# Optimization experiments

Hardware: AMD Instinct MI355X
Metric: run time of the kernel (lower is better)

The kernel has to match this reference:

```python
import jax, jax.numpy as jnp
import numpy as np

HIDDEN = 2048
HEADS = 16
HEAD_DIM = HIDDEN // HEADS  # 128
ROPE_BASE = 10000.0
RMS_EPS = 1e-6
MINUS_INF = -10000.0


def rms_norm(x, w):
    xf = x.astype(jnp.float32)
    var = jnp.mean(xf * xf, axis=-1, keepdims=True)
    return w * (x * jax.lax.rsqrt(var + RMS_EPS))


def rotate_half(x):
    x1, x2 = jnp.split(x, 2, axis=-1)
    return jnp.concatenate((-x2, x1), axis=-1)


def rope_tables(seq_len, dtype):
    inv_freq = 1.0 / (ROPE_BASE ** (jnp.arange(0, HEAD_DIM, 2, dtype=jnp.float32) / HEAD_DIM))
    t = jnp.arange(seq_len, dtype=jnp.float32)
    freqs = jnp.einsum('i,j->ij', t, inv_freq)           # [S, D/2]
    emb = jnp.concatenate((freqs, freqs), axis=-1)       # [S, D]
    return jnp.cos(emb).astype(dtype), jnp.sin(emb).astype(dtype)


def setup_inputs() -> dict:
    key = jax.random.key(0)
    ks = jax.random.split(key, 6)
    B, S, H = 2, 2048, HIDDEN
    x = jax.random.normal(ks[0], (B, S, H), dtype=jnp.float32) * 0.5
    norm_w = jnp.ones((H,), dtype=jnp.float32)
    scale = 0.02
    wq = jax.random.normal(ks[1], (H, H), dtype=jnp.float32) * scale
    wk = jax.random.normal(ks[2], (H, H), dtype=jnp.float32) * scale
    wv = jax.random.normal(ks[3], (H, H), dtype=jnp.float32) * scale
    wo = jax.random.normal(ks[4], (H, H), dtype=jnp.float32) * scale
    position_ids = jnp.broadcast_to(jnp.arange(S, dtype=jnp.int32), (B, S))
    return {"x": x, "norm_w": norm_w, "wq": wq, "wk": wk, "wv": wv,
            "wo": wo, "position_ids": position_ids}


def reference(x, norm_w, wq, wk, wv, wo, position_ids):
    B, S, H = x.shape
    h = rms_norm(x, norm_w)
    # torch Linear: y = h @ W.T, weight is [out, in]
    def proj(w):
        return jnp.einsum('bsd,od->bso', h, w).reshape(B, S, HEADS, HEAD_DIM).transpose(0, 2, 1, 3)
    q, k, v = proj(wq), proj(wk), proj(wv)  # [B, Hh, S, D]
    cos, sin = rope_tables(S, x.dtype)
    cos = cos[position_ids][:, None]  # [B, 1, S, D]
    sin = sin[position_ids][:, None]
    q = q * cos + rotate_half(q) * sin
    k = k * cos + rotate_half(k) * sin
    scores = jnp.einsum('bhqd,bhkd->bhqk', q, k) / jnp.sqrt(jnp.float32(HEAD_DIM))
    causal = jnp.tril(jnp.ones((S, S), dtype=bool))
    scores = scores + jnp.where(causal, 0.0, MINUS_INF).astype(scores.dtype)
    probs = jax.nn.softmax(scores, axis=-1)
    ctx = jnp.einsum('bhqk,bhkd->bhqd', probs, v)          # [B, Hh, S, D]
    ctx = ctx.transpose(0, 2, 1, 3).reshape(B, S, H)
    out = jnp.einsum('bsd,od->bso', ctx, wo)
    return out
```

## Files before the change

kernel.cpp:

```cpp
#include <hip/hip_runtime.h>
#include <hip/hip_bf16.h>
#include <stdint.h>

#define S_LEN   2048
#define BATCH   2
#define HID     2048
#define NHEADS  16
#define HDIM    128
#define ROWS    (BATCH * S_LEN)
#define QS      6144
#define ATT_SCALE 0.08838834764831843f
#define LOG2E     1.4426950408889634f

typedef __attribute__((ext_vector_type(8))) short s16x8;
typedef __attribute__((ext_vector_type(4))) float f32x4;

#define GLL16(gp, lp)                                                          \
  __builtin_amdgcn_global_load_lds(                                            \
      (__attribute__((address_space(1))) void*)(gp),                           \
      (__attribute__((address_space(3))) void*)(lp), 16, 0, 0)

__device__ __forceinline__ float bf2f(unsigned short u) {
  union { unsigned int i; float f; } v; v.i = ((unsigned int)u) << 16; return v.f;
}
__device__ __forceinline__ unsigned short f2bf(float f) {
  union { float f; unsigned int i; } v; v.f = f;
  unsigned int i = v.i;
  return (unsigned short)((i + 0x7FFFu + ((i >> 16) & 1u)) >> 16);
}
__device__ __forceinline__ void store_out(unsigned short* p, float v) { *p = f2bf(v); }
__device__ __forceinline__ void store_out(float* p, float v) { *p = v; }

__global__ __launch_bounds__(256) void cast4_kernel(const float* __restrict__ w0,
                                                    const float* __restrict__ w1,
                                                    const float* __restrict__ w2,
                                                    const float* __restrict__ w3,
                                                    unsigned short* __restrict__ dqkv,
                                                    unsigned short* __restrict__ dwo) {
  const int which = blockIdx.y;
  const float* src = (which == 0) ? w0 : (which == 1) ? w1 : (which == 2) ? w2 : w3;
  unsigned short* dst = (which < 3) ? dqkv + (size_t)which * HID * HID : dwo;
  int i = blockIdx.x * 256 + threadIdx.x;
  float4 v = ((const float4*)src)[i];
  ushort4 o;
  o.x = f2bf(v.x); o.y = f2bf(v.y); o.z = f2bf(v.z); o.w = f2bf(v.w);
  ((ushort4*)dst)[i] = o;
}

__global__ __launch_bounds__(256) void rmsnorm_kernel(const float* __restrict__ x,
                                                      const float* __restrict__ w,
                                                      unsigned short* __restrict__ h) {
  int row = blockIdx.x;
  int t = threadIdx.x;
  const float4* xr4 = (const float4*)(x + (size_t)row * HID);
  float4 a = xr4[t], b = xr4[t + 256];
  float ss = a.x*a.x + a.y*a.y + a.z*a.z + a.w*a.w
           + b.x*b.x + b.y*b.y + b.z*b.z + b.w*b.w;
#pragma unroll
  for (int off = 32; off >= 1; off >>= 1) ss += __shfl_xor(ss, off, 64);
  __shared__ float red[4];
  if ((t & 63) == 0) red[t >> 6] = ss;
  __syncthreads();
  float tot = red[0] + red[1] + red[2] + red[3];
  float rs = rsqrtf(tot * (1.0f / (float)HID) + 1e-6f);
  const float4* w4 = (const float4*)w;
  float4 wa = w4[t], wb = w4[t + 256];
  ushort4 oa, ob;
  oa.x = f2bf(a.x * wa.x * rs); oa.y = f2bf(a.y * wa.y * rs);
  oa.z = f2bf(a.z * wa.z * rs); oa.w = f2bf(a.w * wa.w * rs);
  ob.x = f2bf(b.x * wb.x * rs); ob.y = f2bf(b.y * wb.y * rs);
  ob.z = f2bf(b.z * wb.z * rs); ob.w = f2bf(b.w * wb.w * rs);
  ushort4* hr = (ushort4*)(h + (size_t)row * HID);
  hr[t] = oa; hr[t + 256] = ob;
}

__global__ void rope_tab_kernel(float* __restrict__ cost, float* __restrict__ sint) {
  int s = blockIdx.x, j = threadIdx.x;
  float inv = powf(10000.0f, -((float)j) / 64.0f);
  float ang = (float)s * inv;
  cost[s * 64 + j] = cosf(ang);
  sint[s * 64 + j] = sinf(ang);
}

__global__ __launch_bounds__(256) void rope_kernel(const int* __restrict__ pos_ids,
                                                   const float* __restrict__ cost,
                                                   const float* __restrict__ sint,
                                                   unsigned short* __restrict__ qkv) {
  int row = blockIdx.x;
  int p = pos_ids[row];
  int t = threadIdx.x;
  int head = t >> 4;
  int j0 = (t & 15) * 4;
  size_t base = (size_t)row * QS + head * HDIM;
  float4 c = *(const float4*)(cost + p * 64 + j0);
  float4 s = *(const float4*)(sint + p * 64 + j0);
#pragma unroll
  for (int which = 0; which < 2; which++) {
    unsigned short* ptr = qkv + base + which * HID;
    float sc = which ? 1.0f : (ATT_SCALE * LOG2E);
    ushort4 v1 = *(ushort4*)(ptr + j0);
    ushort4 v2 = *(ushort4*)(ptr + 64 + j0);
    ushort4 o1, o2;
    o1.x = f2bf((bf2f(v1.x) * c.x - bf2f(v2.x) * s.x) * sc);
    o1.y = f2bf((bf2f(v1.y) * c.y - bf2f(v2.y) * s.y) * sc);
    o1.z = f2bf((bf2f(v1.z) * c.z - bf2f(v2.z) * s.z) * sc);
    o1.w = f2bf((bf2f(v1.w) * c.w - bf2f(v2.w) * s.w) * sc);
    o2.x = f2bf((bf2f(v2.x) * c.x + bf2f(v1.x) * s.x) * sc);
    o2.y = f2bf((bf2f(v2.y) * c.y + bf2f(v1.y) * s.y) * sc);
    o2.z = f2bf((bf2f(v2.z) * c.z + bf2f(v1.z) * s.z) * sc);
    o2.w = f2bf((bf2f(v2.w) * c.w + bf2f(v1.w) * s.w) * sc);
    *(ushort4*)(ptr + j0) = o1;
    *(ushort4*)(ptr + 64 + j0) = o2;
  }
}

__global__ __launch_bounds__(256) void transpose_v_kernel(const unsigned short* __restrict__ qkv,
                                                          unsigned short* __restrict__ vt) {
  __shared__ unsigned short tile[64][72];
  const int stile = blockIdx.x, dt = blockIdx.y, bh = blockIdx.z;
  const int t = threadIdx.x;
  const int b = bh >> 4, h = bh & 15;
  const int s0 = stile * 64;
  const unsigned short* src = qkv + (size_t)(b * S_LEN + s0) * QS + 2 * HID + h * HDIM + dt * 64;
#pragma unroll
  for (int it = 0; it < 2; it++) {
    int sl = (t >> 3) + 32 * it;
    int dl = (t & 7) * 8;
    *(s16x8*)&tile[sl][dl] = *(const s16x8*)(src + (size_t)sl * QS + dl);
  }
  __syncthreads();
#pragma unroll
  for (int it = 0; it < 2; it++) {
    int dl = (t >> 3) + 32 * it;
    int sl8 = (t & 7) * 8;
    s16x8 o;
#pragma unroll
    for (int jj = 0; jj < 8; jj++) o[jj] = (short)tile[sl8 + jj][dl];
    *(s16x8*)(vt + (size_t)(bh * 128 + dt * 64 + dl) * S_LEN + s0 + sl8) = o;
  }
}

#define SH(kt, bi, kk2) {                                                      \
    const unsigned short* sa_ = aQ + (size_t)(kt) * 64 + (kk2) * 32;           \
    const unsigned short* sb_ = bQ + (size_t)(kt) * 64 + (kk2) * 32;           \
    char* da_ = qsm + ((bi) * 2 + (kk2)) * 32768 + tid * 16;                   \
    GLL16(sa_, da_);                                                           \
    GLL16(sa_ + (size_t)128 * K, da_ + 8192);                                  \
    GLL16(sb_, da_ + 16384);                                                   \
    GLL16(sb_ + (size_t)128 * K, da_ + 16384 + 8192);                          \
  }

__global__ __launch_bounds__(512, 2) void gemm_qk_kernel(const unsigned short* __restrict__ A,
                                                         const unsigned short* __restrict__ B,
                                                         unsigned short* __restrict__ C,
                                                         int K, int N) {
  __shared__ __align__(16) unsigned short Qsm[2][2][2][256 * 32];
  const int bm = blockIdx.y, bn = blockIdx.x;
  const int tid = threadIdx.x;
  const int w = tid >> 6, wr = w >> 2, wc = w & 3;
  const int l = tid & 63, g = l >> 4, r = l & 15;
  const int KT = K >> 6;

  const int srow = tid >> 2;
  const int sg = (tid & 3) ^ ((tid >> 2) & 3) ^ ((tid >> 4) & 3);
  const unsigned short* aQ = A + (size_t)(bm * 256 + srow) * K + sg * 8;
  const unsigned short* bQ = B + (size_t)(bn * 256 + srow) * K + sg * 8;
  char* const qsm = (char*)Qsm;

  f32x4 zero = {0.f, 0.f, 0.f, 0.f};
  f32x4 acc[8][4];
#pragma unroll
  for (int mi = 0; mi < 8; mi++)
#pragma unroll
    for (int ni = 0; ni < 4; ni++) acc[mi][ni] = zero;

  const int ro = ((g ^ (r & 3) ^ ((r >> 2) & 3)) << 4);
  const int aOff = (wr * 128 + r) * 64 + ro;
  const int bOff = 16384 + (wc * 64 + r) * 64 + ro;

  SH(0, 0, 0); SH(0, 0, 1);

  for (int kt = 0; kt < KT; ++kt) {
    const int buf = kt & 1;
    const bool more = (kt + 1 < KT);
    const char* l0 = qsm + (buf * 2 + 0) * 32768;
    const char* l1 = qsm + (buf * 2 + 1) * 32768;

    asm volatile("s_waitcnt vmcnt(4)" ::: "memory");
    __builtin_amdgcn_s_barrier();
    __builtin_amdgcn_sched_barrier(0);
    s16x8 a[4], b[4];
#pragma unroll
    for (int ni = 0; ni < 4; ni++) b[ni] = *(const s16x8*)(l0 + bOff + ni * 1024);
#pragma unroll
    for (int i = 0; i < 4; i++) a[i] = *(const s16x8*)(l0 + aOff + i * 1024);
    if (more) SH(kt + 1, buf ^ 1, 0);
    __builtin_amdgcn_s_setprio(1);
#pragma unroll
    for (int ni = 0; ni < 4; ni++)
#pragma unroll
      for (int i = 0; i < 4; i++)
        acc[i][ni] = __builtin_amdgcn_mfma_f32_16x16x32_bf16(a[i], b[ni], acc[i][ni], 0, 0, 0);
    __builtin_amdgcn_s_setprio(0);

    s16x8 a2[4];
#pragma unroll
    for (int i = 0; i < 4; i++) a2[i] = *(const s16x8*)(l0 + aOff + (4 + i) * 1024);
    __builtin_amdgcn_s_setprio(1);
#pragma unroll
    for (int ni = 0; ni < 4; ni++)
#pragma unroll
      for (int i = 0; i < 4; i++)
        acc[4 + i][ni] = __builtin_amdgcn_mfma_f32_16x16x32_bf16(a2[i], b[ni], acc[4 + i][ni], 0, 0, 0);
    __builtin_amdgcn_s_setprio(0);

    if (more) { asm volatile("s_waitcnt vmcnt(4)" ::: "memory"); }
    else      { asm volatile("s_waitcnt vmcnt(0)" ::: "memory"); }
    __builtin_amdgcn_s_barrier();
    __builtin_amdgcn_sched_barrier(0);
#pragma unroll
    for (int ni = 0; ni < 4; ni++) b[ni] = *(const s16x8*)(l1 + bOff + ni * 1024);
#pragma unroll
    for (int i = 0; i < 4; i++) a[i] = *(const s16x8*)(l1 + aOff + i * 1024);
    if (more) SH(kt + 1, buf ^ 1, 1);
    __builtin_amdgcn_s_setprio(1);
#pragma unroll
    for (int ni = 0; ni < 4; ni++)
#pragma unroll
      for (int i = 0; i < 4; i++)
        acc[i][ni] = __builtin_amdgcn_mfma_f32_16x16x32_bf16(a[i], b[ni], acc[i][ni], 0, 0, 0);
    __builtin_amdgcn_s_setprio(0);

#pragma unroll
    for (int i = 0; i < 4; i++) a2[i] = *(const s16x8*)(l1 + aOff + (4 + i) * 1024);
    __builtin_amdgcn_s_setprio(1);
#pragma unroll
    for (int ni = 0; ni < 4; ni++)
#pragma unroll
      for (int i = 0; i < 4; i++)
        acc[4 + i][ni] = __builtin_amdgcn_mfma_f32_16x16x32_bf16(a2[i], b[ni], acc[4 + i][ni], 0, 0, 0);
    __builtin_amdgcn_s_setprio(0);
  }

#pragma unroll
  for (int mi = 0; mi < 8; mi++)
#pragma unroll
    for (int ni = 0; ni < 4; ni++) {
      const int crow = bm * 256 + wr * 128 + mi * 16 + g * 4;
      const int ccol = bn * 256 + wc * 64 + ni * 16 + r;
#pragma unroll
      for (int j = 0; j < 4; j++)
        store_out(&C[(size_t)(crow + j) * N + ccol], acc[mi][ni][j]);
    }
}
#undef SH

#define SA(kt, bi) {                                                           \
    const unsigned short* s_ = aS + (size_t)(kt) * 64;                         \
    char* d_ = (char*)Ab[bi] + tid * 16;                                       \
    GLL16(s_, d_);                                                             \
    GLL16(s_ + (size_t)64 * K, d_ + 8192);                                     \
  }
#define SB(kt, bi, hf) {                                                       \
    const unsigned short* s_ = bS + (size_t)(hf) * 128 * K + (size_t)(kt) * 64;\
    char* d_ = (char*)Bb[bi] + (hf) * 16384 + tid * 16;                        \
    GLL16(s_, d_);                                                             \
    GLL16(s_ + (size_t)64 * K, d_ + 8192);                                     \
  }

template <typename OutT, int NI>
__global__ __launch_bounds__(512, 1) void gemm8_kernel(const unsigned short* __restrict__ A,
                                                       const unsigned short* __restrict__ B,
                                                       OutT* __restrict__ C, int K, int N) {
  __shared__ __align__(16) unsigned short Ab[3][128 * 64];
  __shared__ __align__(16) unsigned short Bb[3][NI * 64 * 64];
  const int bm = blockIdx.y, bn = blockIdx.x;
  const int tid = threadIdx.x;
  const int w = tid >> 6, wr = w >> 2, wc = w & 3;
  const int l = tid & 63, g = l >> 4, r = l & 15;
  const int KT = K >> 6;

  const int srow = tid >> 3;
  const int sgr = (tid & 7) ^ (srow & 7);
  const unsigned short* aS = A + (size_t)(bm * 128 + srow) * K + sgr * 8;
  const unsigned short* bS = B + (size_t)(bn * (NI * 64) + srow) * K + sgr * 8;

  f32x4 zero = {0.f, 0.f, 0.f, 0.f};
  f32x4 acc[4][NI];
#pragma unroll
  for (int mi = 0; mi < 4; mi++)
#pragma unroll
    for (int ni = 0; ni < NI; ni++) acc[mi][ni] = zero;

  const int swx = (r & 7) << 4;
  const int ks0 = (g << 4) ^ swx;
  const int ks1 = ((4 | g) << 4) ^ swx;
  const int aOff = (wr * 64 + r) * 128;
  const int bOff = (wc * (NI * 16) + r) * 128;

  SA(0, 0); SB(0, 0, 0); if (NI == 4) SB(0, 0, 1);
  SA(1, 1); SB(1, 1, 0); if (NI == 4) SB(1, 1, 1);

  int cur = 0;
  for (int kt = 0; kt < KT; ++kt) {
    const int b2 = (cur >= 1) ? cur - 1 : cur + 2;
    if (kt == KT - 1)      { asm volatile("s_waitcnt vmcnt(0)" ::: "memory"); }
    else if (NI == 4)      { asm volatile("s_waitcnt vmcnt(6)" ::: "memory"); }
    else                   { asm volatile("s_waitcnt vmcnt(4)" ::: "memory"); }
    __builtin_amdgcn_s_barrier();
    __builtin_amdgcn_sched_barrier(0);
    const char* lA = (const char*)Ab[cur];
    const char* lB = (const char*)Bb[cur];
    const bool more = (kt + 2 < KT);

    s16x8 a[4][2], b[NI][2];
#pragma unroll
    for (int mi = 0; mi < 4; mi++) {
      a[mi][0] = *(const s16x8*)(lA + aOff + mi * 2048 + ks0);
      a[mi][1] = *(const s16x8*)(lA + aOff + mi * 2048 + ks1);
    }
#pragma unroll
    for (int ni = 0; ni < NI / 2; ni++) {
      b[ni][0] = *(const s16x8*)(lB + bOff + ni * 2048 + ks0);
      b[ni][1] = *(const s16x8*)(lB + bOff + ni * 2048 + ks1);
    }
    if (more) { SA(kt + 2, b2); if (NI == 4) SB(kt + 2, b2, 0); }
    __builtin_amdgcn_s_setprio(1);
#pragma unroll
    for (int kk = 0; kk < 2; kk++)
#pragma unroll
      for (int ni = 0; ni < NI / 2; ni++)
#pragma unroll
        for (int mi = 0; mi < 4; mi++)
          acc[mi][ni] = __builtin_amdgcn_mfma_f32_16x16x32_bf16(a[mi][kk], b[ni][kk], acc[mi][ni], 0, 0, 0);
    __builtin_amdgcn_s_setprio(0);
    __builtin_amdgcn_sched_barrier(0);

#pragma unroll
    for (int ni = NI / 2; ni < NI; ni++) {
      b[ni][0] = *(const s16x8*)(lB + bOff + ni * 2048 + ks0);
      b[ni][1] = *(const s16x8*)(lB + bOff + ni * 2048 + ks1);
    }
    if (more) { if (NI == 4) { SB(kt + 2, b2, 1); } else { SB(kt + 2, b2, 0); } }
    __builtin_amdgcn_s_setprio(1);
#pragma unroll
    for (int kk = 0; kk < 2; kk++)
#pragma unroll
      for (int ni = NI / 2; ni < NI; ni++)
#pragma unroll
        for (int mi = 0; mi < 4; mi++)
          acc[mi][ni] = __builtin_amdgcn_mfma_f32_16x16x32_bf16(a[mi][kk], b[ni][kk], acc[mi][ni], 0, 0, 0);
    __builtin_amdgcn_s_setprio(0);
    cur = (cur == 2) ? 0 : cur + 1;
  }

#pragma unroll
  for (int mi = 0; mi < 4; mi++)
#pragma unroll
    for (int ni = 0; ni < NI; ni++) {
      const int crow = bm * 128 + wr * 64 + mi * 16 + g * 4;
      const int ccol = bn * (NI * 64) + wc * (NI * 16) + ni * 16 + r;
#pragma unroll
      for (int j = 0; j < 4; j++)
        store_out(&C[(size_t)(crow + j) * N + ccol], acc[mi][ni][j]);
    }
}

__global__ __launch_bounds__(256, 2) void attn_kernel(const unsigned short* __restrict__ QKV,
                                                      const unsigned short* __restrict__ VT,
                                                      unsigned short* __restrict__ O) {
  __shared__ __align__(16) unsigned short Ksm[2][64 * 128];
  __shared__ __align__(16) unsigned short VTsm[2][128 * 64];
  __shared__ __align__(16) unsigned short Psm[4 * 16 * 64];
  const int bid = blockIdx.x;
  const int grp = bid & 7, idx = bid >> 3;
  const int qt = 31 - (idx >> 2);
  const int bh = (grp << 2) | (idx & 3);
  const int b = bh >> 4, hd = bh & 15;
  const int tid = threadIdx.x, w = tid >> 6, l = tid & 63, g = l >> 4, r = l & 15;
  const int qbs = qt * 64 + w * 16;

  const unsigned short* qp = QKV + (size_t)(b * S_LEN + qbs + r) * QS + hd * HDIM;
  s16x8 qf[4];
#pragma unroll
  for (int ks = 0; ks < 4; ks++) qf[ks] = *(const s16x8*)(qp + ks * 32 + g * 8);

  float mreg[4], lreg[4];
  f32x4 zero = {0.f, 0.f, 0.f, 0.f};
  f32x4 oacc[8];
#pragma unroll
  for (int jj = 0; jj < 4; jj++) { mreg[jj] = -1e30f; lreg[jj] = 0.f; }
#pragma unroll
  for (int di = 0; di < 8; di++) oacc[di] = zero;

  const int cK = tid & 15, rowK = tid >> 4;
  const unsigned short* kp_base = QKV + (size_t)(b * S_LEN + rowK) * QS + HID + hd * HDIM
                                  + ((cK ^ (rowK & 7)) << 3);
  const int cV = tid & 7, dV = tid >> 3;
  const unsigned short* vp_base = VT + (size_t)(bh * 128 + dV) * S_LEN + ((cV ^ (dV & 7)) << 3);
  char* const ksm0 = (char*)Ksm;
  char* const vtsm0 = (char*)VTsm;
  char* const psm_w = (char*)Psm + w * 2048;

#define STAGE(kt, bufi)                                                        \
  {                                                                            \
    const unsigned short* kp_ = kp_base + (size_t)((kt) * 64) * QS;            \
    const unsigned short* vp_ = vp_base + (kt) * 64;                           \
    char* kd_ = ksm0 + (bufi) * 16384;                                         \
    char* vd_ = vtsm0 + (bufi) * 16384;                                        \
    GLL16(kp_,                      kd_ + tid * 16);                           \
    GLL16(kp_ + (size_t)16 * QS,    kd_ + (tid + 256) * 16);                   \
    GLL16(kp_ + (size_t)32 * QS,    kd_ + (tid + 512) * 16);                   \
    GLL16(kp_ + (size_t)48 * QS,    kd_ + (tid + 768) * 16);                   \
    GLL16(vp_,                      vd_ + tid * 16);                           \
    GLL16(vp_ + (size_t)32 * S_LEN, vd_ + (tid + 256) * 16);                   \
    GLL16(vp_ + (size_t)64 * S_LEN, vd_ + (tid + 512) * 16);                   \
    GLL16(vp_ + (size_t)96 * S_LEN, vd_ + (tid + 768) * 16);                   \
  }

  const int nt = qt + 1;
  STAGE(0, 0);

  for (int kt2 = 0; kt2 < nt; kt2++) {
    const int buf = kt2 & 1;
    asm volatile("s_waitcnt vmcnt(0)" ::: "memory");
    __builtin_amdgcn_s_barrier();
    __builtin_amdgcn_sched_barrier(0);
    if (kt2 + 1 < nt) STAGE(kt2 + 1, buf ^ 1);

    const char* ksm_c = ksm0 + buf * 16384;
    const char* vtsm_c = vtsm0 + buf * 16384;

    f32x4 sacc[4];
#pragma unroll
    for (int ni = 0; ni < 4; ni++) sacc[ni] = zero;
#pragma unroll
    for (int ni = 0; ni < 4; ni++) {
      const int krow = ni * 16 + r;
      const int swz = (krow & 7) << 4;
      const char* kb2 = ksm_c + krow * 256;
#pragma unroll
      for (int ks = 0; ks < 4; ks++) {
        s16x8 kf = *(const s16x8*)(kb2 + ((ks * 64 + g * 16) ^ swz));
        sacc[ni] = __builtin_amdgcn_mfma_f32_16x16x32_bf16(qf[ks], kf, sacc[ni], 0, 0, 0);
      }
    }

    if (kt2 == qt) {
#pragma unroll
      for (int ni = 0; ni < 4; ni++)
#pragma unroll
        for (int jj = 0; jj < 4; jj++)
          if ((kt2 * 64 + ni * 16 + r) > (qbs + g * 4 + jj)) sacc[ni][jj] = -1e30f;
    }

    float mrow[4];
#pragma unroll
    for (int jj = 0; jj < 4; jj++)
      mrow[jj] = fmaxf(fmaxf(sacc[0][jj], sacc[1][jj]), fmaxf(sacc[2][jj], sacc[3][jj]));
#pragma unroll
    for (int jj = 0; jj < 4; jj++) {
#pragma unroll
      for (int off = 8; off >= 1; off >>= 1)
        mrow[jj] = fmaxf(mrow[jj], __shfl_xor(mrow[jj], off, 64));
    }
    bool grow = false;
#pragma unroll
    for (int jj = 0; jj < 4; jj++) grow = grow || (mrow[jj] > mreg[jj] + 8.0f);
    if (__any(grow)) {
#pragma unroll
      for (int jj = 0; jj < 4; jj++) {
        float mn = fmaxf(mreg[jj], mrow[jj]);
        float corr = exp2f(mreg[jj] - mn);
        mreg[jj] = mn;
        lreg[jj] *= corr;
#pragma unroll
        for (int di = 0; di < 8; di++) oacc[di][jj] *= corr;
      }
    }
#pragma unroll
    for (int jj = 0; jj < 4; jj++) {
      float sm = 0.f;
#pragma unroll
      for (int ni = 0; ni < 4; ni++) {
        float p2 = exp2f(sacc[ni][jj] - mreg[jj]);
        sacc[ni][jj] = p2;
        sm += p2;
      }
#pragma unroll
      for (int off = 8; off >= 1; off >>= 1) sm += __shfl_xor(sm, off, 64);
      lreg[jj] += sm;
    }

#pragma unroll
    for (int ni = 0; ni < 4; ni++) {
      unsigned int pk01, pk23;
      asm("v_cvt_pk_bf16_f32 %0, %1, %2" : "=v"(pk01) : "v"(sacc[ni][0]), "v"(sacc[ni][1]));
      asm("v_cvt_pk_bf16_f32 %0, %1, %2" : "=v"(pk23) : "v"(sacc[ni][2]), "v"(sacc[ni][3]));
      const int col2 = (ni * 16 + r) << 1;
      const int pr0 = g * 4;
      *(unsigned short*)(psm_w + (((pr0 + 0) * 128 + col2) ^ (((pr0 + 0) & 7) << 4))) = (unsigned short)pk01;
      *(unsigned short*)(psm_w + (((pr0 + 1) * 128 + col2) ^ (((pr0 + 1) & 7) << 4))) = (unsigned short)(pk01 >> 16);
      *(unsigned short*)(psm_w + (((pr0 + 2) * 128 + col2) ^ (((pr0 + 2) & 7) << 4))) = (unsigned short)pk23;
      *(unsigned short*)(psm_w + (((pr0 + 3) * 128 + col2) ^ (((pr0 + 3) & 7) << 4))) = (unsigned short)(pk23 >> 16);
    }

#pragma unroll
    for (int ksl = 0; ksl < 2; ksl++) {
      s16x8 pa = *(const s16x8*)(psm_w + ((r * 128 + ((ksl * 32 + g * 8) << 1)) ^ ((r & 7) << 4)));
      const int kgran = ksl * 4 + g;
#pragma unroll
      for (int di = 0; di < 8; di++) {
        const int d = di * 16 + r;
        s16x8 vf = *(const s16x8*)(vtsm_c + d * 128 + ((kgran ^ (d & 7)) << 4));
        oacc[di] = __builtin_amdgcn_mfma_f32_16x16x32_bf16(pa, vf, oacc[di], 0, 0, 0);
      }
    }
  }
#undef STAGE

#pragma unroll
  for (int di = 0; di < 8; di++)
#pragma unroll
    for (int jj = 0; jj < 4; jj++) {
      int orow = qbs + g * 4 + jj;
      O[(size_t)(b * S_LEN + orow) * HID + hd * HDIM + di * 16 + r] =
          f2bf(oacc[di][jj] / lreg[jj]);
    }
}

extern "C" void kernel_launch(void* const* d_in, const int* in_sizes, int n_in,
                              void* d_out, int out_size, void* d_ws, size_t ws_size,
                              hipStream_t stream) {
  const float* x      = (const float*)d_in[0];
  const float* norm_w = (const float*)d_in[1];
  const float* wq     = (const float*)d_in[2];
  const float* wk     = (const float*)d_in[3];
  const float* wv     = (const float*)d_in[4];
  const float* wo     = (const float*)d_in[5];
  const int*   pos    = (const int*)d_in[6];
  float* out = (float*)d_out;

  char* ws = (char*)d_ws;
  const size_t WQKV_B = (size_t)3 * HID * HID * 2;
  const size_t WO_B   = (size_t)HID * HID * 2;
  const size_t H_B    = (size_t)ROWS * HID * 2;
  const size_t QKV_B  = (size_t)ROWS * QS * 2;

  unsigned short* wqkvb = (unsigned short*)(ws);
  unsigned short* vt    = (unsigned short*)(ws);
  unsigned short* wob   = (unsigned short*)(ws + WQKV_B);
  unsigned short* h     = (unsigned short*)(ws + WQKV_B + WO_B);
  unsigned short* qkv   = (unsigned short*)(ws + WQKV_B + WO_B + H_B);
  float* cost = (float*)(ws + WQKV_B + WO_B + H_B + QKV_B);
  float* sint = cost + (size_t)S_LEN * 64;

  dim3 cgrid(HID * HID / 4 / 256, 4);
  cast4_kernel<<<cgrid, 256, 0, stream>>>(wq, wk, wv, wo, wqkvb, wob);
  rope_tab_kernel<<<S_LEN, 64, 0, stream>>>(cost, sint);
  rmsnorm_kernel<<<ROWS, 256, 0, stream>>>(x, norm_w, h);

  dim3 qkgrid(2 * HID / 256, ROWS / 256);
  gemm_qk_kernel<<<qkgrid, 512, 0, stream>>>(h, wqkvb, qkv, HID, QS);

  dim3 vgrid(HID / 256, ROWS / 128);
  gemm8_kernel<unsigned short, 4><<<vgrid, 512, 0, stream>>>(
      h, wqkvb + (size_t)2 * HID * HID, qkv + 2 * HID, HID, QS);

  dim3 tgrid(S_LEN / 64, 2, BATCH * NHEADS);
  transpose_v_kernel<<<tgrid, 256, 0, stream>>>(qkv, vt);

  rope_kernel<<<ROWS, 256, 0, stream>>>(pos, cost, sint, qkv);

  attn_kernel<<<1024, 256, 0, stream>>>(qkv, vt, h );

  dim3 ogrid(HID / 256, ROWS / 128);
  gemm8_kernel<float, 4><<<ogrid, 512, 0, stream>>>(h, wob, out, HID, HID);
}
```

Measured before the change: 284.6 us.

## Fuse V transpose into V GEMM epilogue and transpose attention MFMA layout

The V projection GEMM now writes its output directly in the transposed [b,h,d,s] layout, which removes the separate transpose kernel and the round trip of V through the QKV buffer. The QKV buffer shrinks to Q and K only. The attention kernel swaps MFMA operand order so each lane owns one query row. That lets row max and row sum reductions use two shuffles and one scalar per lane instead of four, makes P writes into shared memory packed 32-bit stores, and makes output stores vectorized. The cost is that the V GEMM epilogue writes scattered 8-byte stores, and V now overlaps the weight buffer in the workspace, so ordering across kernels matters.

```diff
diff --git a/kernel.cpp b/kernel.cpp
--- a/kernel.cpp
+++ b/kernel.cpp
@@ -8,7 +8,7 @@
 #define NHEADS  16
 #define HDIM    128
 #define ROWS    (BATCH * S_LEN)
-#define QS      6144
+#define QKS     4096
 #define ATT_SCALE 0.08838834764831843f
 #define LOG2E     1.4426950408889634f
 
@@ -85,18 +85,18 @@
 __global__ __launch_bounds__(256) void rope_kernel(const int* __restrict__ pos_ids,
                                                    const float* __restrict__ cost,
                                                    const float* __restrict__ sint,
-                                                   unsigned short* __restrict__ qkv) {
+                                                   unsigned short* __restrict__ qk) {
   int row = blockIdx.x;
   int p = pos_ids[row];
   int t = threadIdx.x;
   int head = t >> 4;
   int j0 = (t & 15) * 4;
-  size_t base = (size_t)row * QS + head * HDIM;
+  size_t base = (size_t)row * QKS + head * HDIM;
   float4 c = *(const float4*)(cost + p * 64 + j0);
   float4 s = *(const float4*)(sint + p * 64 + j0);
 #pragma unroll
   for (int which = 0; which < 2; which++) {
-    unsigned short* ptr = qkv + base + which * HID;
+    unsigned short* ptr = qk + base + which * HID;
     float sc = which ? 1.0f : (ATT_SCALE * LOG2E);
     ushort4 v1 = *(ushort4*)(ptr + j0);
     ushort4 v2 = *(ushort4*)(ptr + 64 + j0);
@@ -114,32 +114,6 @@
   }
 }
 
-__global__ __launch_bounds__(256) void transpose_v_kernel(const unsigned short* __restrict__ qkv,
-                                                          unsigned short* __restrict__ vt) {
-  __shared__ unsigned short tile[64][72];
-  const int stile = blockIdx.x, dt = blockIdx.y, bh = blockIdx.z;
-  const int t = threadIdx.x;
-  const int b = bh >> 4, h = bh & 15;
-  const int s0 = stile * 64;
-  const unsigned short* src = qkv + (size_t)(b * S_LEN + s0) * QS + 2 * HID + h * HDIM + dt * 64;
-#pragma unroll
-  for (int it = 0; it < 2; it++) {
-    int sl = (t >> 3) + 32 * it;
-    int dl = (t & 7) * 8;
-    *(s16x8*)&tile[sl][dl] = *(const s16x8*)(src + (size_t)sl * QS + dl);
-  }
-  __syncthreads();
-#pragma unroll
-  for (int it = 0; it < 2; it++) {
-    int dl = (t >> 3) + 32 * it;
-    int sl8 = (t & 7) * 8;
-    s16x8 o;
-#pragma unroll
-    for (int jj = 0; jj < 8; jj++) o[jj] = (short)tile[sl8 + jj][dl];
-    *(s16x8*)(vt + (size_t)(bh * 128 + dt * 64 + dl) * S_LEN + s0 + sl8) = o;
-  }
-}
-
 #define SH(kt, bi, kk2) {                                                      \
     const unsigned short* sa_ = aQ + (size_t)(kt) * 64 + (kk2) * 32;           \
     const unsigned short* sb_ = bQ + (size_t)(kt) * 64 + (kk2) * 32;           \
@@ -268,7 +242,7 @@
     GLL16(s_ + (size_t)64 * K, d_ + 8192);                                     \
   }
 
-template <typename OutT, int NI>
+template <typename OutT, int NI, bool VT_OUT>
 __global__ __launch_bounds__(512, 1) void gemm8_kernel(const unsigned short* __restrict__ A,
                                                        const unsigned short* __restrict__ B,
                                                        OutT* __restrict__ C, int K, int N) {
@@ -360,13 +334,23 @@
     for (int ni = 0; ni < NI; ni++) {
       const int crow = bm * 128 + wr * 64 + mi * 16 + g * 4;
       const int ccol = bn * (NI * 64) + wc * (NI * 16) + ni * 16 + r;
-#pragma unroll
-      for (int j = 0; j < 4; j++)
-        store_out(&C[(size_t)(crow + j) * N + ccol], acc[mi][ni][j]);
-    }
-}
-
-__global__ __launch_bounds__(256, 2) void attn_kernel(const unsigned short* __restrict__ QKV,
+      if constexpr (VT_OUT) {
+        const int bidx = crow >> 11;
+        const int s0 = crow & (S_LEN - 1);
+        const int vrow = (bidx * 16 + (ccol >> 7)) * 128 + (ccol & 127);
+        ushort4 o;
+        o.x = f2bf(acc[mi][ni][0]); o.y = f2bf(acc[mi][ni][1]);
+        o.z = f2bf(acc[mi][ni][2]); o.w = f2bf(acc[mi][ni][3]);
+        *(ushort4*)((unsigned short*)C + (size_t)vrow * S_LEN + s0) = o;
+      } else {
+#pragma unroll
+        for (int j = 0; j < 4; j++)
+          store_out(&C[(size_t)(crow + j) * N + ccol], acc[mi][ni][j]);
+      }
+    }
+}
+
+__global__ __launch_bounds__(256, 2) void attn_kernel(const unsigned short* __restrict__ QK,
                                                       const unsigned short* __restrict__ VT,
                                                       unsigned short* __restrict__ O) {
   __shared__ __align__(16) unsigned short Ksm[2][64 * 128];
@@ -380,38 +364,37 @@
   const int tid = threadIdx.x, w = tid >> 6, l = tid & 63, g = l >> 4, r = l & 15;
   const int qbs = qt * 64 + w * 16;
 
-  const unsigned short* qp = QKV + (size_t)(b * S_LEN + qbs + r) * QS + hd * HDIM;
+  const unsigned short* qp = QK + (size_t)(b * S_LEN + qbs + r) * QKS + hd * HDIM;
   s16x8 qf[4];
 #pragma unroll
   for (int ks = 0; ks < 4; ks++) qf[ks] = *(const s16x8*)(qp + ks * 32 + g * 8);
 
-  float mreg[4], lreg[4];
+  float mreg = -1e30f, lreg = 0.f;
   f32x4 zero = {0.f, 0.f, 0.f, 0.f};
   f32x4 oacc[8];
 #pragma unroll
-  for (int jj = 0; jj < 4; jj++) { mreg[jj] = -1e30f; lreg[jj] = 0.f; }
-#pragma unroll
   for (int di = 0; di < 8; di++) oacc[di] = zero;
 
   const int cK = tid & 15, rowK = tid >> 4;
-  const unsigned short* kp_base = QKV + (size_t)(b * S_LEN + rowK) * QS + HID + hd * HDIM
+  const unsigned short* kp_base = QK + (size_t)(b * S_LEN + rowK) * QKS + HID + hd * HDIM
                                   + ((cK ^ (rowK & 7)) << 3);
   const int cV = tid & 7, dV = tid >> 3;
   const unsigned short* vp_base = VT + (size_t)(bh * 128 + dV) * S_LEN + ((cV ^ (dV & 7)) << 3);
   char* const ksm0 = (char*)Ksm;
   char* const vtsm0 = (char*)VTsm;
   char* const psm_w = (char*)Psm + w * 2048;
+  const int pswz = (r & 7) << 4;
 
 #define STAGE(kt, bufi)                                                        \
   {                                                                            \
-    const unsigned short* kp_ = kp_base + (size_t)((kt) * 64) * QS;            \
+    const unsigned short* kp_ = kp_base + (size_t)((kt) * 64) * QKS;           \
     const unsigned short* vp_ = vp_base + (kt) * 64;                           \
     char* kd_ = ksm0 + (bufi) * 16384;                                         \
     char* vd_ = vtsm0 + (bufi) * 16384;                                        \
     GLL16(kp_,                      kd_ + tid * 16);                           \
-    GLL16(kp_ + (size_t)16 * QS,    kd_ + (tid + 256) * 16);                   \
-    GLL16(kp_ + (size_t)32 * QS,    kd_ + (tid + 512) * 16);                   \
-    GLL16(kp_ + (size_t)48 * QS,    kd_ + (tid + 768) * 16);                   \
+    GLL16(kp_ + (size_t)16 * QKS,   kd_ + (tid + 256) * 16);                   \
+    GLL16(kp_ + (size_t)32 * QKS,   kd_ + (tid + 512) * 16);                   \
+    GLL16(kp_ + (size_t)48 * QKS,   kd_ + (tid + 768) * 16);                   \
     GLL16(vp_,                      vd_ + tid * 16);                           \
     GLL16(vp_ + (size_t)32 * S_LEN, vd_ + (tid + 256) * 16);                   \
     GLL16(vp_ + (size_t)64 * S_LEN, vd_ + (tid + 512) * 16);                   \
@@ -442,7 +425,7 @@
 #pragma unroll
       for (int ks = 0; ks < 4; ks++) {
         s16x8 kf = *(const s16x8*)(kb2 + ((ks * 64 + g * 16) ^ swz));
-        sacc[ni] = __builtin_amdgcn_mfma_f32_16x16x32_bf16(qf[ks], kf, sacc[ni], 0, 0, 0);
+        sacc[ni] = __builtin_amdgcn_mfma_f32_16x16x32_bf16(kf, qf[ks], sacc[ni], 0, 0, 0);
       }
     }
 
@@ -451,82 +434,72 @@
       for (int ni = 0; ni < 4; ni++)
 #pragma unroll
         for (int jj = 0; jj < 4; jj++)
-          if ((kt2 * 64 + ni * 16 + r) > (qbs + g * 4 + jj)) sacc[ni][jj] = -1e30f;
-    }
-
-    float mrow[4];
-#pragma unroll
-    for (int jj = 0; jj < 4; jj++)
-      mrow[jj] = fmaxf(fmaxf(sacc[0][jj], sacc[1][jj]), fmaxf(sacc[2][jj], sacc[3][jj]));
-#pragma unroll
-    for (int jj = 0; jj < 4; jj++) {
-#pragma unroll
-      for (int off = 8; off >= 1; off >>= 1)
-        mrow[jj] = fmaxf(mrow[jj], __shfl_xor(mrow[jj], off, 64));
-    }
-    bool grow = false;
-#pragma unroll
-    for (int jj = 0; jj < 4; jj++) grow = grow || (mrow[jj] > mreg[jj] + 8.0f);
-    if (__any(grow)) {
-#pragma unroll
-      for (int jj = 0; jj < 4; jj++) {
-        float mn = fmaxf(mreg[jj], mrow[jj]);
-        float corr = exp2f(mreg[jj] - mn);
-        mreg[jj] = mn;
-        lreg[jj] *= corr;
-#pragma unroll
-        for (int di = 0; di < 8; di++) oacc[di][jj] *= corr;
-      }
-    }
-#pragma unroll
-    for (int jj = 0; jj < 4; jj++) {
-      float sm = 0.f;
-#pragma unroll
-      for (int ni = 0; ni < 4; ni++) {
-        float p2 = exp2f(sacc[ni][jj] - mreg[jj]);
-        sacc[ni][jj] = p2;
-        sm += p2;
-      }
-#pragma unroll
-      for (int off = 8; off >= 1; off >>= 1) sm += __shfl_xor(sm, off, 64);
-      lreg[jj] += sm;
-    }
+          if ((kt2 * 64 + ni * 16 + g * 4 + jj) > (qbs + r)) sacc[ni][jj] = -1e30f;
+    }
+
+    float m0 = fmaxf(fmaxf(sacc[0][0], sacc[0][1]), fmaxf(sacc[0][2], sacc[0][3]));
+    float m1 = fmaxf(fmaxf(sacc[1][0], sacc[1][1]), fmaxf(sacc[1][2], sacc[1][3]));
+    float m2 = fmaxf(fmaxf(sacc[2][0], sacc[2][1]), fmaxf(sacc[2][2], sacc[2][3]));
+    float m3 = fmaxf(fmaxf(sacc[3][0], sacc[3][1]), fmaxf(sacc[3][2], sacc[3][3]));
+    float mx = fmaxf(fmaxf(m0, m1), fmaxf(m2, m3));
+    mx = fmaxf(mx, __shfl_xor(mx, 16, 64));
+    mx = fmaxf(mx, __shfl_xor(mx, 32, 64));
+
+    if (__any(mx > mreg + 8.0f)) {
+      float mn = fmaxf(mreg, mx);
+      float corr = exp2f(mreg - mn);
+      mreg = mn;
+      lreg *= corr;
+#pragma unroll
+      for (int di = 0; di < 8; di++) oacc[di] = oacc[di] * corr;
+    }
+
+#pragma unroll
+    for (int ni = 0; ni < 4; ni++)
+#pragma unroll
+      for (int jj = 0; jj < 4; jj++) sacc[ni][jj] = exp2f(sacc[ni][jj] - mreg);
+    float s0 = (sacc[0][0] + sacc[0][1]) + (sacc[0][2] + sacc[0][3]);
+    float s1 = (sacc[1][0] + sacc[1][1]) + (sacc[1][2] + sacc[1][3]);
+    float s2 = (sacc[2][0] + sacc[2][1]) + (sacc[2][2] + sacc[2][3]);
+    float s3 = (sacc[3][0] + sacc[3][1]) + (sacc[3][2] + sacc[3][3]);
+    float sm = (s0 + s1) + (s2 + s3);
+    sm += __shfl_xor(sm, 16, 64);
+    sm += __shfl_xor(sm, 32, 64);
+    lreg += sm;
 
 #pragma unroll
     for (int ni = 0; ni < 4; ni++) {
       unsigned int pk01, pk23;
       asm("v_cvt_pk_bf16_f32 %0, %1, %2" : "=v"(pk01) : "v"(sacc[ni][0]), "v"(sacc[ni][1]));
       asm("v_cvt_pk_bf16_f32 %0, %1, %2" : "=v"(pk23) : "v"(sacc[ni][2]), "v"(sacc[ni][3]));
-      const int col2 = (ni * 16 + r) << 1;
-      const int pr0 = g * 4;
-      *(unsigned short*)(psm_w + (((pr0 + 0) * 128 + col2) ^ (((pr0 + 0) & 7) << 4))) = (unsigned short)pk01;
-      *(unsigned short*)(psm_w + (((pr0 + 1) * 128 + col2) ^ (((pr0 + 1) & 7) << 4))) = (unsigned short)(pk01 >> 16);
-      *(unsigned short*)(psm_w + (((pr0 + 2) * 128 + col2) ^ (((pr0 + 2) & 7) << 4))) = (unsigned short)pk23;
-      *(unsigned short*)(psm_w + (((pr0 + 3) * 128 + col2) ^ (((pr0 + 3) & 7) << 4))) = (unsigned short)(pk23 >> 16);
+      const int byte0 = (r * 128 + ni * 32 + g * 8) ^ pswz;
+      *(unsigned int*)(psm_w + byte0) = pk01;
+      *(unsigned int*)(psm_w + byte0 + 4) = pk23;
     }
 
 #pragma unroll
     for (int ksl = 0; ksl < 2; ksl++) {
-      s16x8 pa = *(const s16x8*)(psm_w + ((r * 128 + ((ksl * 32 + g * 8) << 1)) ^ ((r & 7) << 4)));
+      s16x8 pb = *(const s16x8*)(psm_w + ((r * 128 + ksl * 64 + g * 16) ^ pswz));
       const int kgran = ksl * 4 + g;
 #pragma unroll
       for (int di = 0; di < 8; di++) {
         const int d = di * 16 + r;
         s16x8 vf = *(const s16x8*)(vtsm_c + d * 128 + ((kgran ^ (d & 7)) << 4));
-        oacc[di] = __builtin_amdgcn_mfma_f32_16x16x32_bf16(pa, vf, oacc[di], 0, 0, 0);
+        oacc[di] = __builtin_amdgcn_mfma_f32_16x16x32_bf16(vf, pb, oacc[di], 0, 0, 0);
       }
     }
   }
 #undef STAGE
 
-#pragma unroll
-  for (int di = 0; di < 8; di++)
-#pragma unroll
-    for (int jj = 0; jj < 4; jj++) {
-      int orow = qbs + g * 4 + jj;
-      O[(size_t)(b * S_LEN + orow) * HID + hd * HDIM + di * 16 + r] =
-          f2bf(oacc[di][jj] / lreg[jj]);
-    }
+  const float inv = 1.0f / lreg;
+  unsigned short* orow = O + (size_t)(b * S_LEN + qbs + r) * HID + hd * HDIM;
+#pragma unroll
+  for (int di = 0; di < 8; di++) {
+    ushort4 o;
+    o.x = f2bf(oacc[di][0] * inv); o.y = f2bf(oacc[di][1] * inv);
+    o.z = f2bf(oacc[di][2] * inv); o.w = f2bf(oacc[di][3] * inv);
+    *(ushort4*)(orow + di * 16 + g * 4) = o;
+  }
 }
 
 extern "C" void kernel_launch(void* const* d_in, const int* in_sizes, int n_in,
@@ -545,14 +518,14 @@
   const size_t WQKV_B = (size_t)3 * HID * HID * 2;
   const size_t WO_B   = (size_t)HID * HID * 2;
   const size_t H_B    = (size_t)ROWS * HID * 2;
-  const size_t QKV_B  = (size_t)ROWS * QS * 2;
+  const size_t QK_B   = (size_t)ROWS * QKS * 2;
 
   unsigned short* wqkvb = (unsigned short*)(ws);
   unsigned short* vt    = (unsigned short*)(ws);
   unsigned short* wob   = (unsigned short*)(ws + WQKV_B);
   unsigned short* h     = (unsigned short*)(ws + WQKV_B + WO_B);
-  unsigned short* qkv   = (unsigned short*)(ws + WQKV_B + WO_B + H_B);
-  float* cost = (float*)(ws + WQKV_B + WO_B + H_B + QKV_B);
+  unsigned short* qk    = (unsigned short*)(ws + WQKV_B + WO_B + H_B);
+  float* cost = (float*)(ws + WQKV_B + WO_B + H_B + QK_B);
   float* sint = cost + (size_t)S_LEN * 64;
 
   dim3 cgrid(HID * HID / 4 / 256, 4);
@@ -561,19 +534,16 @@
   rmsnorm_kernel<<<ROWS, 256, 0, stream>>>(x, norm_w, h);
 
   dim3 qkgrid(2 * HID / 256, ROWS / 256);
-  gemm_qk_kernel<<<qkgrid, 512, 0, stream>>>(h, wqkvb, qkv, HID, QS);
+  gemm_qk_kernel<<<qkgrid, 512, 0, stream>>>(h, wqkvb, qk, HID, QKS);
 
   dim3 vgrid(HID / 256, ROWS / 128);
-  gemm8_kernel<unsigned short, 4><<<vgrid, 512, 0, stream>>>(
-      h, wqkvb + (size_t)2 * HID * HID, qkv + 2 * HID, HID, QS);
-
-  dim3 tgrid(S_LEN / 64, 2, BATCH * NHEADS);
-  transpose_v_kernel<<<tgrid, 256, 0, stream>>>(qkv, vt);
-
-  rope_kernel<<<ROWS, 256, 0, stream>>>(pos, cost, sint, qkv);
-
-  attn_kernel<<<1024, 256, 0, stream>>>(qkv, vt, h );
+  gemm8_kernel<unsigned short, 4, true><<<vgrid, 512, 0, stream>>>(
+      h, wqkvb + (size_t)2 * HID * HID, vt, HID, S_LEN);
+
+  rope_kernel<<<ROWS, 256, 0, stream>>>(pos, cost, sint, qk);
+
+  attn_kernel<<<1024, 256, 0, stream>>>(qk, vt, h );
 
   dim3 ogrid(HID / 256, ROWS / 128);
-  gemm8_kernel<float, 4><<<ogrid, 512, 0, stream>>>(h, wob, out, HID, HID);
-}
+  gemm8_kernel<float, 4, false><<<ogrid, 512, 0, stream>>>(h, wob, out, HID, HID);
+}
```

Measured after the change: 256.2 us. -10.0%, faster.
